# Optimization experiments

Hardware: AMD Instinct MI355X
Metric: run time of the kernel (lower is better)

Reference implementation:

```python
import jax, jax.numpy as jnp
import numpy as np

T = 8192        # total tokens
D = 2048        # hidden size
I = 2048        # intermediate dim
E = 8           # num experts
K = 2           # num_experts_per_tok


def setup_inputs() -> dict:
    key = jax.random.key(0)
    k1, k2, k3, k4, k5 = jax.random.split(key, 5)
    return {
        "inputs": jax.random.normal(k1, (T, D), dtype=jnp.float32),
        "router_logits": jax.random.normal(k2, (T, E), dtype=jnp.float32),
        "wi_0": jax.random.normal(k3, (E, D, I), dtype=jnp.float32) * 0.02,
        "wi_1": jax.random.normal(k4, (E, D, I), dtype=jnp.float32) * 0.02,
        "wo": jax.random.normal(k5, (E, I, D), dtype=jnp.float32) * 0.02,
    }


def reference(inputs, router_logits, wi_0, wi_1, wo):
    total_tokens, hidden = inputs.shape
    num_experts = router_logits.shape[-1]
    dtype = inputs.dtype

    # --- router: top-k, softmax over selected logits, renormalize ---
    top_k_logits, top_k_indices = jax.lax.top_k(router_logits, K)     # [T,K]
    top_k_weights = jax.nn.softmax(top_k_logits.astype(jnp.float32), axis=-1).astype(dtype)
    top_k_weights = top_k_weights / jnp.sum(top_k_weights, axis=-1, keepdims=True)

    # --- permute: replicate each token K times, sort token-expert pairs by expert id ---
    flat_experts = top_k_indices.reshape(-1)                          # [T*K]
    sort_idx = jnp.argsort(flat_experts)                              # stable sort -> grouped by expert
    x_rep = jnp.repeat(inputs, K, axis=0)                             # [T*K, D]
    x_sorted = x_rep[sort_idx]                                        # [T*K, D] grouped per expert
    group_sizes = jnp.bincount(flat_experts, length=num_experts).astype(jnp.int32)  # [E]

    # --- grouped GEMM (ragged_dot) over contiguous expert groups: SwiGLU FFN ---
    h0 = jax.lax.ragged_dot(x_sorted, wi_0, group_sizes, preferred_element_type=dtype)
    h1 = jax.lax.ragged_dot(x_sorted, wi_1, group_sizes, preferred_element_type=dtype)
    inter = jax.nn.silu(h0) * h1                                      # [T*K, I]
    out_sorted = jax.lax.ragged_dot(inter, wo, group_sizes, preferred_element_type=dtype)  # [T*K, D]

    # --- unpermute + weighted combine ---
    inv_idx = jnp.argsort(sort_idx)
    out_pairs = out_sorted[inv_idx].reshape(total_tokens, K, hidden)  # [T,K,D]
    output = jnp.einsum("tkd,tk->td", out_pairs, top_k_weights)       # [T,D]
    return output
```

## Files before the change

kernel.cpp:

```cpp
#include <hip/hip_runtime.h>
#include <hip/hip_bf16.h>
#include <stdint.h>

#define T_TOK 8192
#define DDIM 2048
#define IDIM 2048
#define NEXP 8
#define NPAIR (T_TOK*2)
#define MAXROWS (NPAIR + NEXP*128)
#define MAXTILES (MAXROWS/128)

typedef __attribute__((ext_vector_type(8))) short short8;
typedef __attribute__((ext_vector_type(4))) float f32x4;

__device__ __forceinline__ ushort f2bf(float f) {
  union { float f; unsigned int u; } v; v.f = f;
  unsigned int u = v.u;
  unsigned int r = (u + 0x7fffu + ((u >> 16) & 1u)) >> 16;
  return (ushort)r;
}

__device__ __forceinline__ void glds16(const void* g, void* l) {
  __builtin_amdgcn_global_load_lds(
      (const __attribute__((address_space(1))) unsigned int*)g,
      (__attribute__((address_space(3))) unsigned int*)l, 16, 0, 0);
}

__global__ void router_kernel(const float* __restrict__ logits, int* __restrict__ pair_e,
                              float* __restrict__ pair_w, int* __restrict__ cnt) {
  __shared__ int c[NEXP];
  int tid = threadIdx.x;
  int t = blockIdx.x * 256 + tid;
  if (tid < NEXP) c[tid] = 0;
  __syncthreads();
  float lv[NEXP];
  #pragma unroll
  for (int e = 0; e < NEXP; ++e) lv[e] = logits[t * NEXP + e];
  int i0 = 0;
  #pragma unroll
  for (int e = 1; e < NEXP; ++e) if (lv[e] > lv[i0]) i0 = e;
  int i1 = (i0 == 0) ? 1 : 0;
  #pragma unroll
  for (int e = 0; e < NEXP; ++e) if (e != i0 && lv[e] > lv[i1]) i1 = e;
  float ex = __expf(lv[i1] - lv[i0]);
  float w1 = ex / (1.f + ex);
  float w0 = 1.f - w1;
  pair_e[2*t] = i0; pair_e[2*t+1] = i1;
  pair_w[2*t] = w0; pair_w[2*t+1] = w1;
  atomicAdd(&c[i0], 1); atomicAdd(&c[i1], 1);
  __syncthreads();
  if (tid < NEXP) atomicAdd(&cnt[tid], c[tid]);
}

__global__ void scan_kernel(const int* __restrict__ cnt, int* __restrict__ poff) {
  if (threadIdx.x == 0 && blockIdx.x == 0) {
    int o = 0; poff[0] = 0;
    for (int e = 0; e < NEXP; ++e) { o += (cnt[e] + 127) & ~127; poff[e+1] = o; }
  }
}

__global__ void scatter_kernel(const int* __restrict__ pair_e, const float* __restrict__ pair_w,
                               const int* __restrict__ poff, int* __restrict__ fill,
                               int* __restrict__ row_token, float* __restrict__ row_weight) {
  __shared__ int lc[NEXP], lb[NEXP];
  int tid = threadIdx.x;
  int t = blockIdx.x * 256 + tid;
  if (tid < NEXP) lc[tid] = 0;
  __syncthreads();
  int e0 = pair_e[2*t], e1 = pair_e[2*t+1];
  int r0 = atomicAdd(&lc[e0], 1);
  int r1 = atomicAdd(&lc[e1], 1);
  __syncthreads();
  if (tid < NEXP) lb[tid] = atomicAdd(&fill[tid], lc[tid]);
  __syncthreads();
  int p0 = poff[e0] + lb[e0] + r0;
  int p1 = poff[e1] + lb[e1] + r1;
  row_token[p0] = t; row_weight[p0] = pair_w[2*t];
  row_token[p1] = t; row_weight[p1] = pair_w[2*t+1];
}

__global__ void convert_x_kernel(const float* __restrict__ x, ushort* __restrict__ xb) {
  size_t i = ((size_t)blockIdx.x * 256 + threadIdx.x) * 8;
  float4 a = *(const float4*)(x + i);
  float4 b = *(const float4*)(x + i + 4);
  uint4 o;
  o.x = (unsigned)f2bf(a.x) | ((unsigned)f2bf(a.y) << 16);
  o.y = (unsigned)f2bf(a.z) | ((unsigned)f2bf(a.w) << 16);
  o.z = (unsigned)f2bf(b.x) | ((unsigned)f2bf(b.y) << 16);
  o.w = (unsigned)f2bf(b.z) | ((unsigned)f2bf(b.w) << 16);
  *(uint4*)(xb + i) = o;
}

__global__ void transpose_w_kernel(const float* __restrict__ wi0, const float* __restrict__ wi1,
                                   const float* __restrict__ wo, ushort* __restrict__ w0t,
                                   ushort* __restrict__ w1t, ushort* __restrict__ wot) {
  int mz = blockIdx.z;
  int mat = mz >> 3, e = mz & 7;
  const float* src = (mat == 0 ? wi0 : (mat == 1 ? wi1 : wo)) + (size_t)e * DDIM * IDIM;
  ushort* dst = (mat == 0 ? w0t : (mat == 1 ? w1t : wot)) + (size_t)e * DDIM * IDIM;
  __shared__ ushort tbuf[64][72];
  int tid = threadIdx.x;
  int bi = blockIdx.x, bj = blockIdx.y;
  int rl = tid >> 4;
  int cl = (tid & 15) * 4;
  #pragma unroll
  for (int it = 0; it < 4; ++it) {
    int r = rl + it * 16;
    float4 v = *(const float4*)(src + (size_t)(bi*64 + r) * 2048 + bj*64 + cl);
    tbuf[cl+0][r] = f2bf(v.x);
    tbuf[cl+1][r] = f2bf(v.y);
    tbuf[cl+2][r] = f2bf(v.z);
    tbuf[cl+3][r] = f2bf(v.w);
  }
  __syncthreads();
  int n = tid >> 2, ch = tid & 3;
  const ushort* p = &tbuf[n][ch*16];
  unsigned pk[8];
  #pragma unroll
  for (int j = 0; j < 8; ++j) pk[j] = (unsigned)p[2*j] | ((unsigned)p[2*j+1] << 16);
  ushort* d = dst + (size_t)(bj*64 + n) * 2048 + bi*64 + ch*16;
  uint4 o0, o1;
  o0.x = pk[0]; o0.y = pk[1]; o0.z = pk[2]; o0.w = pk[3];
  o1.x = pk[4]; o1.y = pk[5]; o1.z = pk[6]; o1.w = pk[7];
  *(uint4*)(d) = o0;
  *(uint4*)(d + 8) = o1;
}

__global__ __launch_bounds__(256, 2) void gemm1_kernel(
    const ushort* __restrict__ xb, const ushort* __restrict__ w0t,
    const ushort* __restrict__ w1t, const int* __restrict__ row_token,
    const int* __restrict__ poff, ushort* __restrict__ inter) {
  const int rt = blockIdx.x, ct = blockIdx.y;
  const int row0 = rt * 128;
  if (row0 >= poff[NEXP]) return;
  int e = 0;
  #pragma unroll
  for (int i = 1; i < NEXP; ++i) e += (row0 >= poff[i]);

  __shared__ __align__(16) char smem[2 * 24576];
  const int tid = threadIdx.x;
  const int w = tid >> 6, l = tid & 63;

  const ushort* aSrc[2]; const ushort* b0Src[2]; const ushort* b1Src[2];
  int ldsOff[2];
  #pragma unroll
  for (int c = 0; c < 2; ++c) {
    int o = c * 4096 + w * 1024 + l * 16;
    int m = o >> 6;
    int ci = (o >> 4) & 3;
    int kl = ((ci ^ ((m >> 1) & 3)) << 3);
    ldsOff[c] = c * 4096 + w * 1024;
    int tok = row_token[row0 + m];
    aSrc[c]  = xb  + (size_t)tok * DDIM + kl;
    int n = ct * 128 + m;
    b0Src[c] = w0t + ((size_t)e * IDIM + n) * DDIM + kl;
    b1Src[c] = w1t + ((size_t)e * IDIM + n) * DDIM + kl;
  }

  f32x4 acc0[4][4], acc1[4][4];
  #pragma unroll
  for (int i = 0; i < 4; ++i)
    #pragma unroll
    for (int j = 0; j < 4; ++j) { acc0[i][j] = (f32x4)(0.f); acc1[i][j] = (f32x4)(0.f); }

  const int wr = w >> 1, wc = w & 1;
  const int fr = l & 15, kq = l >> 4;
  int aOff[4], bOff[4];
  #pragma unroll
  for (int mi = 0; mi < 4; ++mi) {
    int m = wr * 64 + mi * 16 + fr;
    aOff[mi] = m * 64 + ((kq * 16) ^ (((m >> 1) & 3) << 4));
  }
  #pragma unroll
  for (int ni = 0; ni < 4; ++ni) {
    int n = wc * 64 + ni * 16 + fr;
    bOff[ni] = n * 64 + ((kq * 16) ^ (((n >> 1) & 3) << 4));
  }

  const int NT = DDIM / 32;
  #pragma unroll
  for (int c = 0; c < 2; ++c) {
    glds16(aSrc[c],  smem + 0     + ldsOff[c]);
    glds16(b0Src[c], smem + 8192  + ldsOff[c]);
    glds16(b1Src[c], smem + 16384 + ldsOff[c]);
  }
  __syncthreads();

  int buf = 0;
  for (int kt = 0; kt < NT; ++kt) {
    if (kt + 1 < NT) {
      char* base = smem + (buf ^ 1) * 24576;
      int kadv = (kt + 1) * 32;
      #pragma unroll
      for (int c = 0; c < 2; ++c) {
        glds16(aSrc[c]  + kadv, base + 0     + ldsOff[c]);
        glds16(b0Src[c] + kadv, base + 8192  + ldsOff[c]);
        glds16(b1Src[c] + kadv, base + 16384 + ldsOff[c]);
      }
    }
    const char* cb = smem + buf * 24576;
    short8 a[4], b0[4], b1[4];
    #pragma unroll
    for (int mi = 0; mi < 4; ++mi) a[mi] = *(const short8*)(cb + aOff[mi]);
    #pragma unroll
    for (int ni = 0; ni < 4; ++ni) {
      b0[ni] = *(const short8*)(cb + 8192  + bOff[ni]);
      b1[ni] = *(const short8*)(cb + 16384 + bOff[ni]);
    }
    #pragma unroll
    for (int mi = 0; mi < 4; ++mi)
      #pragma unroll
      for (int ni = 0; ni < 4; ++ni) {
        acc0[mi][ni] = __builtin_amdgcn_mfma_f32_16x16x32_bf16(a[mi], b0[ni], acc0[mi][ni], 0, 0, 0);
        acc1[mi][ni] = __builtin_amdgcn_mfma_f32_16x16x32_bf16(a[mi], b1[ni], acc1[mi][ni], 0, 0, 0);
      }
    __syncthreads();
    buf ^= 1;
  }

  #pragma unroll
  for (int mi = 0; mi < 4; ++mi)
    #pragma unroll
    for (int ni = 0; ni < 4; ++ni) {
      int col = ct * 128 + wc * 64 + ni * 16 + fr;
      #pragma unroll
      for (int j = 0; j < 4; ++j) {
        int row = row0 + wr * 64 + mi * 16 + kq * 4 + j;
        float h0 = acc0[mi][ni][j];
        float h1 = acc1[mi][ni][j];
        float s = h0 / (1.f + __expf(-h0));
        inter[(size_t)row * IDIM + col] = f2bf(s * h1);
      }
    }
}

__global__ __launch_bounds__(256, 2) void gemm2_kernel(
    const ushort* __restrict__ inter, const ushort* __restrict__ wot,
    const int* __restrict__ row_token, const float* __restrict__ row_weight,
    const int* __restrict__ poff, float* __restrict__ dout) {
  const int rt = blockIdx.x, ct = blockIdx.y;
  const int row0 = rt * 128;
  if (row0 >= poff[NEXP]) return;
  int e = 0;
  #pragma unroll
  for (int i = 1; i < NEXP; ++i) e += (row0 >= poff[i]);

  __shared__ __align__(16) char smem[2 * 16384];
  __shared__ int tok_s[128];
  __shared__ float wgt_s[128];
  const int tid = threadIdx.x;
  if (tid < 128) { tok_s[tid] = row_token[row0 + tid]; wgt_s[tid] = row_weight[row0 + tid]; }

  const int w = tid >> 6, l = tid & 63;
  const ushort* aSrc[2]; const ushort* bSrc[2];
  int ldsOff[2];
  #pragma unroll
  for (int c = 0; c < 2; ++c) {
    int o = c * 4096 + w * 1024 + l * 16;
    int m = o >> 6;
    int ci = (o >> 4) & 3;
    int kl = ((ci ^ ((m >> 1) & 3)) << 3);
    ldsOff[c] = c * 4096 + w * 1024;
    aSrc[c] = inter + (size_t)(row0 + m) * IDIM + kl;
    bSrc[c] = wot + ((size_t)e * DDIM + ct * 128 + m) * IDIM + kl;
  }

  f32x4 acc[4][4];
  #pragma unroll
  for (int i = 0; i < 4; ++i)
    #pragma unroll
    for (int j = 0; j < 4; ++j) acc[i][j] = (f32x4)(0.f);

  const int wr = w >> 1, wc = w & 1;
  const int fr = l & 15, kq = l >> 4;
  int aOff[4], bOff[4];
  #pragma unroll
  for (int mi = 0; mi < 4; ++mi) {
    int m = wr * 64 + mi * 16 + fr;
    aOff[mi] = m * 64 + ((kq * 16) ^ (((m >> 1) & 3) << 4));
  }
  #pragma unroll
  for (int ni = 0; ni < 4; ++ni) {
    int n = wc * 64 + ni * 16 + fr;
    bOff[ni] = n * 64 + ((kq * 16) ^ (((n >> 1) & 3) << 4));
  }

  const int NT = IDIM / 32;
  #pragma unroll
  for (int c = 0; c < 2; ++c) {
    glds16(aSrc[c], smem + 0    + ldsOff[c]);
    glds16(bSrc[c], smem + 8192 + ldsOff[c]);
  }
  __syncthreads();

  int buf = 0;
  for (int kt = 0; kt < NT; ++kt) {
    if (kt + 1 < NT) {
      char* base = smem + (buf ^ 1) * 16384;
      int kadv = (kt + 1) * 32;
      #pragma unroll
      for (int c = 0; c < 2; ++c) {
        glds16(aSrc[c] + kadv, base + 0    + ldsOff[c]);
        glds16(bSrc[c] + kadv, base + 8192 + ldsOff[c]);
      }
    }
    const char* cb = smem + buf * 16384;
    short8 a[4], b[4];
    #pragma unroll
    for (int mi = 0; mi < 4; ++mi) a[mi] = *(const short8*)(cb + aOff[mi]);
    #pragma unroll
    for (int ni = 0; ni < 4; ++ni) b[ni] = *(const short8*)(cb + 8192 + bOff[ni]);
    #pragma unroll
    for (int mi = 0; mi < 4; ++mi)
      #pragma unroll
      for (int ni = 0; ni < 4; ++ni)
        acc[mi][ni] = __builtin_amdgcn_mfma_f32_16x16x32_bf16(a[mi], b[ni], acc[mi][ni], 0, 0, 0);
    __syncthreads();
    buf ^= 1;
  }

  #pragma unroll
  for (int mi = 0; mi < 4; ++mi)
    #pragma unroll
    for (int ni = 0; ni < 4; ++ni) {
      int col = ct * 128 + wc * 64 + ni * 16 + fr;
      #pragma unroll
      for (int j = 0; j < 4; ++j) {
        int rl2 = wr * 64 + mi * 16 + kq * 4 + j;
        float wv = wgt_s[rl2];
        if (wv != 0.f) {
          int t = tok_s[rl2];
          atomicAdd(&dout[(size_t)t * DDIM + col], wv * acc[mi][ni][j]);
        }
      }
    }
}

extern "C" void kernel_launch(void* const* d_in, const int* in_sizes, int n_in,
                              void* d_out, int out_size, void* d_ws, size_t ws_size,
                              hipStream_t stream) {
  const float* x   = (const float*)d_in[0];
  const float* rl  = (const float*)d_in[1];
  const float* wi0 = (const float*)d_in[2];
  const float* wi1 = (const float*)d_in[3];
  const float* wo  = (const float*)d_in[4];
  float* out = (float*)d_out;

  char* ws = (char*)d_ws;
  ushort* xb    = (ushort*)(ws);
  ushort* w0t   = (ushort*)(ws + 33554432ull);
  ushort* w1t   = (ushort*)(ws + 100663296ull);
  ushort* wot   = (ushort*)(ws + 167772160ull);
  ushort* inter = (ushort*)(ws + 234881024ull);
  char* ctrl    = ws + 306184192ull;
  int*   row_token  = (int*)(ctrl);
  float* row_weight = (float*)(ctrl + 69632);
  int*   cnt   = (int*)(ctrl + 139264);
  int*   fill  = (int*)(ctrl + 139296);
  int*   poff  = (int*)(ctrl + 139328);
  int*   pair_e = (int*)(ctrl + 139392);
  float* pair_w = (float*)(ctrl + 204928);

  hipMemsetAsync(ctrl, 0, 139328, stream);
  router_kernel<<<T_TOK/256, 256, 0, stream>>>(rl, pair_e, pair_w, cnt);
  scan_kernel<<<1, 64, 0, stream>>>(cnt, poff);
  scatter_kernel<<<T_TOK/256, 256, 0, stream>>>(pair_e, pair_w, poff, fill, row_token, row_weight);
  convert_x_kernel<<<(T_TOK*DDIM)/(256*8), 256, 0, stream>>>(x, xb);
  transpose_w_kernel<<<dim3(32, 32, 24), 256, 0, stream>>>(wi0, wi1, wo, w0t, w1t, wot);
  hipMemsetAsync(d_out, 0, (size_t)out_size * sizeof(float), stream);
  gemm1_kernel<<<dim3(MAXTILES, 16), 256, 0, stream>>>(xb, w0t, w1t, row_token, poff, inter);
  gemm2_kernel<<<dim3(MAXTILES, 16), 256, 0, stream>>>(inter, wot, row_token, row_weight, poff, out);
}
```

Baseline: 1.092 ms.

## Enlarge GEMM tiles to 256 rows with 512 threads and software-pipelined staging

Both grouped GEMMs move to 256-row tiles with 8 waves, 64-wide K steps, a larger LDS double buffer and staged async loads interleaved with MFMA phases under fine-grained vmcnt waits and s_setprio. Expert padding grows to 256 rows and the grid is reordered so column tiles vary fastest, which is meant to improve operand reuse and overlap loads with compute. The wo transpose is deferred until after gemm1 and reuses the w0t buffer, which shrinks the workspace. The costs are more padding rows, 128KB of LDS per block, and fragile hand-written barrier and waitcnt scheduling.

```diff
diff --git a/kernel.cpp b/kernel.cpp
--- a/kernel.cpp
+++ b/kernel.cpp
@@ -7,8 +7,9 @@
 #define IDIM 2048
 #define NEXP 8
 #define NPAIR (T_TOK*2)
-#define MAXROWS (NPAIR + NEXP*128)
-#define MAXTILES (MAXROWS/128)
+#define MAXROWS (NPAIR + NEXP*256)
+#define RTILES (MAXROWS/256)
+#define NTK 32
 
 typedef __attribute__((ext_vector_type(8))) short short8;
 typedef __attribute__((ext_vector_type(4))) float f32x4;
@@ -25,6 +26,11 @@
       (const __attribute__((address_space(1))) unsigned int*)g,
       (__attribute__((address_space(3))) unsigned int*)l, 16, 0, 0);
 }
+
+#define BAR() __builtin_amdgcn_s_barrier()
+#define VMC6() asm volatile("s_waitcnt vmcnt(6)" ::: "memory")
+#define VMC4() asm volatile("s_waitcnt vmcnt(4)" ::: "memory")
+#define VMC0() asm volatile("s_waitcnt vmcnt(0)" ::: "memory")
 
 __global__ void router_kernel(const float* __restrict__ logits, int* __restrict__ pair_e,
                               float* __restrict__ pair_w, int* __restrict__ cnt) {
@@ -55,7 +61,7 @@
 __global__ void scan_kernel(const int* __restrict__ cnt, int* __restrict__ poff) {
   if (threadIdx.x == 0 && blockIdx.x == 0) {
     int o = 0; poff[0] = 0;
-    for (int e = 0; e < NEXP; ++e) { o += (cnt[e] + 127) & ~127; poff[e+1] = o; }
+    for (int e = 0; e < NEXP; ++e) { o += (cnt[e] + 255) & ~255; poff[e+1] = o; }
   }
 }
 
@@ -91,13 +97,12 @@
   *(uint4*)(xb + i) = o;
 }
 
-__global__ void transpose_w_kernel(const float* __restrict__ wi0, const float* __restrict__ wi1,
-                                   const float* __restrict__ wo, ushort* __restrict__ w0t,
-                                   ushort* __restrict__ w1t, ushort* __restrict__ wot) {
+__global__ void transpose_w_kernel(const float* __restrict__ s0, ushort* __restrict__ d0,
+                                   const float* __restrict__ s1, ushort* __restrict__ d1) {
   int mz = blockIdx.z;
   int mat = mz >> 3, e = mz & 7;
-  const float* src = (mat == 0 ? wi0 : (mat == 1 ? wi1 : wo)) + (size_t)e * DDIM * IDIM;
-  ushort* dst = (mat == 0 ? w0t : (mat == 1 ? w1t : wot)) + (size_t)e * DDIM * IDIM;
+  const float* src = (mat ? s1 : s0) + (size_t)e * DDIM * IDIM;
+  ushort* dst = (mat ? d1 : d0) + (size_t)e * DDIM * IDIM;
   __shared__ ushort tbuf[64][72];
   int tid = threadIdx.x;
   int bi = blockIdx.x, bj = blockIdx.y;
@@ -126,211 +131,221 @@
   *(uint4*)(d + 8) = o1;
 }
 
-__global__ __launch_bounds__(256, 2) void gemm1_kernel(
+__global__ __launch_bounds__(512, 2) void gemm1_kernel(
     const ushort* __restrict__ xb, const ushort* __restrict__ w0t,
     const ushort* __restrict__ w1t, const int* __restrict__ row_token,
     const int* __restrict__ poff, ushort* __restrict__ inter) {
-  const int rt = blockIdx.x, ct = blockIdx.y;
-  const int row0 = rt * 128;
+  const int ct = blockIdx.x;
+  const int rt = blockIdx.y;
+  const int row0 = rt * 256;
   if (row0 >= poff[NEXP]) return;
   int e = 0;
   #pragma unroll
   for (int i = 1; i < NEXP; ++i) e += (row0 >= poff[i]);
 
-  __shared__ __align__(16) char smem[2 * 24576];
+  __shared__ __align__(16) char sm[131072];
   const int tid = threadIdx.x;
   const int w = tid >> 6, l = tid & 63;
-
-  const ushort* aSrc[2]; const ushort* b0Src[2]; const ushort* b1Src[2];
-  int ldsOff[2];
-  #pragma unroll
-  for (int c = 0; c < 2; ++c) {
-    int o = c * 4096 + w * 1024 + l * 16;
-    int m = o >> 6;
-    int ci = (o >> 4) & 3;
-    int kl = ((ci ^ ((m >> 1) & 3)) << 3);
-    ldsOff[c] = c * 4096 + w * 1024;
-    int tok = row_token[row0 + m];
-    aSrc[c]  = xb  + (size_t)tok * DDIM + kl;
-    int n = ct * 128 + m;
-    b0Src[c] = w0t + ((size_t)e * IDIM + n) * DDIM + kl;
-    b1Src[c] = w1t + ((size_t)e * IDIM + n) * DDIM + kl;
-  }
-
-  f32x4 acc0[4][4], acc1[4][4];
-  #pragma unroll
-  for (int i = 0; i < 4; ++i)
-    #pragma unroll
-    for (int j = 0; j < 4; ++j) { acc0[i][j] = (f32x4)(0.f); acc1[i][j] = (f32x4)(0.f); }
-
-  const int wr = w >> 1, wc = w & 1;
+  const int wr = w >> 2, wc = w & 3;
   const int fr = l & 15, kq = l >> 4;
-  int aOff[4], bOff[4];
-  #pragma unroll
-  for (int mi = 0; mi < 4; ++mi) {
-    int m = wr * 64 + mi * 16 + fr;
-    aOff[mi] = m * 64 + ((kq * 16) ^ (((m >> 1) & 3) << 4));
-  }
-  #pragma unroll
-  for (int ni = 0; ni < 4; ++ni) {
-    int n = wc * 64 + ni * 16 + fr;
-    bOff[ni] = n * 64 + ((kq * 16) ^ (((n >> 1) & 3) << 4));
-  }
-
-  const int NT = DDIM / 32;
-  #pragma unroll
-  for (int c = 0; c < 2; ++c) {
-    glds16(aSrc[c],  smem + 0     + ldsOff[c]);
-    glds16(b0Src[c], smem + 8192  + ldsOff[c]);
-    glds16(b1Src[c], smem + 16384 + ldsOff[c]);
-  }
-  __syncthreads();
-
-  int buf = 0;
-  for (int kt = 0; kt < NT; ++kt) {
-    if (kt + 1 < NT) {
-      char* base = smem + (buf ^ 1) * 24576;
-      int kadv = (kt + 1) * 32;
-      #pragma unroll
-      for (int c = 0; c < 2; ++c) {
-        glds16(aSrc[c]  + kadv, base + 0     + ldsOff[c]);
-        glds16(b0Src[c] + kadv, base + 8192  + ldsOff[c]);
-        glds16(b1Src[c] + kadv, base + 16384 + ldsOff[c]);
-      }
+
+  const int mloc = tid >> 3;
+  const int kl = ((tid & 7) ^ (mloc & 7)) << 3;
+  const ushort* aP[2][2]; const ushort* b0P[2]; const ushort* b1P[2];
+  #pragma unroll
+  for (int h = 0; h < 2; ++h)
+    #pragma unroll
+    for (int li = 0; li < 2; ++li) {
+      int tok = row_token[row0 + h*128 + li*64 + mloc];
+      aP[h][li] = xb + (size_t)tok * DDIM + kl;
     }
-    const char* cb = smem + buf * 24576;
-    short8 a[4], b0[4], b1[4];
-    #pragma unroll
-    for (int mi = 0; mi < 4; ++mi) a[mi] = *(const short8*)(cb + aOff[mi]);
-    #pragma unroll
-    for (int ni = 0; ni < 4; ++ni) {
-      b0[ni] = *(const short8*)(cb + 8192  + bOff[ni]);
-      b1[ni] = *(const short8*)(cb + 16384 + bOff[ni]);
-    }
-    #pragma unroll
-    for (int mi = 0; mi < 4; ++mi)
-      #pragma unroll
-      for (int ni = 0; ni < 4; ++ni) {
-        acc0[mi][ni] = __builtin_amdgcn_mfma_f32_16x16x32_bf16(a[mi], b0[ni], acc0[mi][ni], 0, 0, 0);
-        acc1[mi][ni] = __builtin_amdgcn_mfma_f32_16x16x32_bf16(a[mi], b1[ni], acc1[mi][ni], 0, 0, 0);
-      }
-    __syncthreads();
-    buf ^= 1;
-  }
-
-  #pragma unroll
-  for (int mi = 0; mi < 4; ++mi)
-    #pragma unroll
-    for (int ni = 0; ni < 4; ++ni) {
-      int col = ct * 128 + wc * 64 + ni * 16 + fr;
+  #pragma unroll
+  for (int li = 0; li < 2; ++li) {
+    int n = ct*128 + li*64 + mloc;
+    b0P[li] = w0t + ((size_t)e * IDIM + n) * DDIM + kl;
+    b1P[li] = w1t + ((size_t)e * IDIM + n) * DDIM + kl;
+  }
+  const int dOff = tid * 16;
+
+#define S_A(h, dd, tt) do { int ka = (tt)*64; char* db = sm + (dd)*65536 + (h)*16384 + dOff; \
+  glds16(aP[h][0] + ka, db); glds16(aP[h][1] + ka, db + 8192); } while(0)
+#define S_B0(dd, tt) do { int ka = (tt)*64; char* db = sm + (dd)*65536 + 32768 + dOff; \
+  glds16(b0P[0] + ka, db); glds16(b0P[1] + ka, db + 8192); } while(0)
+#define S_B1(dd, tt) do { int ka = (tt)*64; char* db = sm + (dd)*65536 + 49152 + dOff; \
+  glds16(b1P[0] + ka, db); glds16(b1P[1] + ka, db + 8192); } while(0)
+
+  const int pc0 = ((kq ^ (fr & 7)) << 4);
+  const int pc1 = (((4 + kq) ^ (fr & 7)) << 4);
+  const int aBase = wr*16384 + fr*128;
+  const int bBase = 32768 + (wc*32 + fr)*128;
+
+#define RD_A(mq) do { const char* p_ = cur + aBase + (mq)*8192; \
+  _Pragma("unroll") for (int mi = 0; mi < 4; ++mi) { \
+    a[mi][0] = *(const short8*)(p_ + mi*2048 + pc0); \
+    a[mi][1] = *(const short8*)(p_ + mi*2048 + pc1); } } while(0)
+#define RD_B(dst_, gg) do { const char* p_ = cur + bBase + (gg)*16384; \
+  _Pragma("unroll") for (int ni = 0; ni < 2; ++ni) { \
+    dst_[ni][0] = *(const short8*)(p_ + ni*2048 + pc0); \
+    dst_[ni][1] = *(const short8*)(p_ + ni*2048 + pc1); } } while(0)
+#define MM(accv, mq, bb) do { __builtin_amdgcn_s_setprio(1); \
+  _Pragma("unroll") for (int mi = 0; mi < 4; ++mi) \
+  _Pragma("unroll") for (int ni = 0; ni < 2; ++ni) { \
+    accv[(mq)*4+mi][ni] = __builtin_amdgcn_mfma_f32_16x16x32_bf16(a[mi][0], bb[ni][0], accv[(mq)*4+mi][ni], 0,0,0); \
+    accv[(mq)*4+mi][ni] = __builtin_amdgcn_mfma_f32_16x16x32_bf16(a[mi][1], bb[ni][1], accv[(mq)*4+mi][ni], 0,0,0); } \
+  __builtin_amdgcn_s_setprio(0); } while(0)
+
+  f32x4 acc0[8][2], acc1[8][2];
+  #pragma unroll
+  for (int i = 0; i < 8; ++i)
+    #pragma unroll
+    for (int j = 0; j < 2; ++j) { acc0[i][j] = (f32x4)(0.f); acc1[i][j] = (f32x4)(0.f); }
+  short8 a[4][2], b0v[2][2], b1v[2][2];
+
+  S_A(0,0,0); S_A(1,0,0); S_B0(0,0); S_B1(0,0);
+  S_B0(1,1); S_B1(1,1); S_A(0,1,1);
+  VMC6(); BAR();
+
+  for (int t = 0; t < NTK; ++t) {
+    const char* cur = sm + (t & 1) * 65536;
+    const int d = t & 1;
+    RD_A(0); RD_B(b0v, 0);
+    if (t+1 < NTK) S_A(1, d^1, t+1);
+    BAR(); MM(acc0, 0, b0v); BAR();
+    RD_B(b1v, 1);
+    if (t+2 < NTK) S_B0(d, t+2);
+    BAR(); MM(acc1, 0, b1v); BAR();
+    RD_A(1);
+    if (t+2 < NTK) S_B1(d, t+2);
+    BAR(); MM(acc1, 1, b1v); BAR();
+    if (t+2 < NTK) { S_A(0, d, t+2); VMC6(); } else { VMC0(); }
+    BAR(); MM(acc0, 1, b0v); BAR();
+  }
+#undef S_A
+#undef S_B0
+#undef S_B1
+#undef RD_A
+#undef RD_B
+#undef MM
+
+  #pragma unroll
+  for (int ai = 0; ai < 8; ++ai)
+    #pragma unroll
+    for (int ni = 0; ni < 2; ++ni) {
+      int col = ct*128 + wc*32 + ni*16 + fr;
       #pragma unroll
       for (int j = 0; j < 4; ++j) {
-        int row = row0 + wr * 64 + mi * 16 + kq * 4 + j;
-        float h0 = acc0[mi][ni][j];
-        float h1 = acc1[mi][ni][j];
+        int row = row0 + wr*128 + ai*16 + kq*4 + j;
+        float h0 = acc0[ai][ni][j], h1 = acc1[ai][ni][j];
         float s = h0 / (1.f + __expf(-h0));
         inter[(size_t)row * IDIM + col] = f2bf(s * h1);
       }
     }
 }
 
-__global__ __launch_bounds__(256, 2) void gemm2_kernel(
+__global__ __launch_bounds__(512, 2) void gemm2_kernel(
     const ushort* __restrict__ inter, const ushort* __restrict__ wot,
     const int* __restrict__ row_token, const float* __restrict__ row_weight,
     const int* __restrict__ poff, float* __restrict__ dout) {
-  const int rt = blockIdx.x, ct = blockIdx.y;
-  const int row0 = rt * 128;
+  const int ct = blockIdx.x;
+  const int rt = blockIdx.y;
+  const int row0 = rt * 256;
   if (row0 >= poff[NEXP]) return;
   int e = 0;
   #pragma unroll
   for (int i = 1; i < NEXP; ++i) e += (row0 >= poff[i]);
 
-  __shared__ __align__(16) char smem[2 * 16384];
-  __shared__ int tok_s[128];
-  __shared__ float wgt_s[128];
+  __shared__ __align__(16) char sm[131072];
+  __shared__ int tok_s[256];
+  __shared__ float wgt_s[256];
   const int tid = threadIdx.x;
-  if (tid < 128) { tok_s[tid] = row_token[row0 + tid]; wgt_s[tid] = row_weight[row0 + tid]; }
+  if (tid < 256) { tok_s[tid] = row_token[row0 + tid]; wgt_s[tid] = row_weight[row0 + tid]; }
 
   const int w = tid >> 6, l = tid & 63;
-  const ushort* aSrc[2]; const ushort* bSrc[2];
-  int ldsOff[2];
-  #pragma unroll
-  for (int c = 0; c < 2; ++c) {
-    int o = c * 4096 + w * 1024 + l * 16;
-    int m = o >> 6;
-    int ci = (o >> 4) & 3;
-    int kl = ((ci ^ ((m >> 1) & 3)) << 3);
-    ldsOff[c] = c * 4096 + w * 1024;
-    aSrc[c] = inter + (size_t)(row0 + m) * IDIM + kl;
-    bSrc[c] = wot + ((size_t)e * DDIM + ct * 128 + m) * IDIM + kl;
-  }
-
-  f32x4 acc[4][4];
-  #pragma unroll
-  for (int i = 0; i < 4; ++i)
+  const int wr = w >> 2, wc = w & 3;
+  const int fr = l & 15, kq = l >> 4;
+
+  const int mloc = tid >> 3;
+  const int kl = ((tid & 7) ^ (mloc & 7)) << 3;
+  const ushort* aP[2][2]; const ushort* bP[2][2];
+  #pragma unroll
+  for (int h = 0; h < 2; ++h)
+    #pragma unroll
+    for (int li = 0; li < 2; ++li) {
+      aP[h][li] = inter + (size_t)(row0 + h*128 + li*64 + mloc) * IDIM + kl;
+      int n = ct*256 + h*128 + li*64 + mloc;
+      bP[h][li] = wot + ((size_t)e * DDIM + n) * IDIM + kl;
+    }
+  const int dOff = tid * 16;
+
+#define S_A2(h, dd, tt) do { int ka = (tt)*64; char* db = sm + (dd)*65536 + (h)*16384 + dOff; \
+  glds16(aP[h][0] + ka, db); glds16(aP[h][1] + ka, db + 8192); } while(0)
+#define S_B2(h, dd, tt) do { int ka = (tt)*64; char* db = sm + (dd)*65536 + 32768 + (h)*16384 + dOff; \
+  glds16(bP[h][0] + ka, db); glds16(bP[h][1] + ka, db + 8192); } while(0)
+
+  const int pc0 = ((kq ^ (fr & 7)) << 4);
+  const int pc1 = (((4 + kq) ^ (fr & 7)) << 4);
+  const int aBase = wr*16384 + fr*128;
+  const int bBase = 32768 + (wc>>1)*16384 + ((wc&1)*64 + fr)*128;
+
+#define RD_A2(mq) do { const char* p_ = cur + aBase + (mq)*8192; \
+  _Pragma("unroll") for (int mi = 0; mi < 4; ++mi) { \
+    a[mi][0] = *(const short8*)(p_ + mi*2048 + pc0); \
+    a[mi][1] = *(const short8*)(p_ + mi*2048 + pc1); } } while(0)
+#define RD_B2(dst_, nq) do { const char* p_ = cur + bBase + (nq)*4096; \
+  _Pragma("unroll") for (int ni = 0; ni < 2; ++ni) { \
+    dst_[ni][0] = *(const short8*)(p_ + ni*2048 + pc0); \
+    dst_[ni][1] = *(const short8*)(p_ + ni*2048 + pc1); } } while(0)
+#define MM2(mq, nq, bb) do { __builtin_amdgcn_s_setprio(1); \
+  _Pragma("unroll") for (int mi = 0; mi < 4; ++mi) \
+  _Pragma("unroll") for (int ni = 0; ni < 2; ++ni) { \
+    acc[(mq)*4+mi][(nq)*2+ni] = __builtin_amdgcn_mfma_f32_16x16x32_bf16(a[mi][0], bb[ni][0], acc[(mq)*4+mi][(nq)*2+ni], 0,0,0); \
+    acc[(mq)*4+mi][(nq)*2+ni] = __builtin_amdgcn_mfma_f32_16x16x32_bf16(a[mi][1], bb[ni][1], acc[(mq)*4+mi][(nq)*2+ni], 0,0,0); } \
+  __builtin_amdgcn_s_setprio(0); } while(0)
+
+  f32x4 acc[8][4];
+  #pragma unroll
+  for (int i = 0; i < 8; ++i)
     #pragma unroll
     for (int j = 0; j < 4; ++j) acc[i][j] = (f32x4)(0.f);
-
-  const int wr = w >> 1, wc = w & 1;
-  const int fr = l & 15, kq = l >> 4;
-  int aOff[4], bOff[4];
-  #pragma unroll
-  for (int mi = 0; mi < 4; ++mi) {
-    int m = wr * 64 + mi * 16 + fr;
-    aOff[mi] = m * 64 + ((kq * 16) ^ (((m >> 1) & 3) << 4));
-  }
-  #pragma unroll
-  for (int ni = 0; ni < 4; ++ni) {
-    int n = wc * 64 + ni * 16 + fr;
-    bOff[ni] = n * 64 + ((kq * 16) ^ (((n >> 1) & 3) << 4));
-  }
-
-  const int NT = IDIM / 32;
-  #pragma unroll
-  for (int c = 0; c < 2; ++c) {
-    glds16(aSrc[c], smem + 0    + ldsOff[c]);
-    glds16(bSrc[c], smem + 8192 + ldsOff[c]);
-  }
-  __syncthreads();
-
-  int buf = 0;
-  for (int kt = 0; kt < NT; ++kt) {
-    if (kt + 1 < NT) {
-      char* base = smem + (buf ^ 1) * 16384;
-      int kadv = (kt + 1) * 32;
-      #pragma unroll
-      for (int c = 0; c < 2; ++c) {
-        glds16(aSrc[c] + kadv, base + 0    + ldsOff[c]);
-        glds16(bSrc[c] + kadv, base + 8192 + ldsOff[c]);
-      }
-    }
-    const char* cb = smem + buf * 16384;
-    short8 a[4], b[4];
-    #pragma unroll
-    for (int mi = 0; mi < 4; ++mi) a[mi] = *(const short8*)(cb + aOff[mi]);
-    #pragma unroll
-    for (int ni = 0; ni < 4; ++ni) b[ni] = *(const short8*)(cb + 8192 + bOff[ni]);
-    #pragma unroll
-    for (int mi = 0; mi < 4; ++mi)
-      #pragma unroll
-      for (int ni = 0; ni < 4; ++ni)
-        acc[mi][ni] = __builtin_amdgcn_mfma_f32_16x16x32_bf16(a[mi], b[ni], acc[mi][ni], 0, 0, 0);
-    __syncthreads();
-    buf ^= 1;
-  }
-
-  #pragma unroll
-  for (int mi = 0; mi < 4; ++mi)
-    #pragma unroll
-    for (int ni = 0; ni < 4; ++ni) {
-      int col = ct * 128 + wc * 64 + ni * 16 + fr;
+  short8 a[4][2], bv0[2][2], bv1[2][2];
+
+  S_A2(0,0,0); S_A2(1,0,0); S_B2(0,0,0); S_B2(1,0,0);
+  S_B2(0,1,1); S_B2(1,1,1);
+  VMC4(); BAR();
+
+  for (int t = 0; t < NTK; ++t) {
+    const char* cur = sm + (t & 1) * 65536;
+    const int d = t & 1;
+    RD_A2(0); RD_B2(bv0, 0);
+    if (t+1 < NTK) S_A2(0, d^1, t+1);
+    BAR(); MM2(0, 0, bv0); BAR();
+    RD_B2(bv1, 1);
+    if (t+1 < NTK) S_A2(1, d^1, t+1);
+    BAR(); MM2(0, 1, bv1); BAR();
+    RD_A2(1);
+    if (t+2 < NTK) S_B2(0, d, t+2);
+    BAR(); MM2(1, 1, bv1); BAR();
+    if (t+2 < NTK) { S_B2(1, d, t+2); VMC4(); } else { VMC0(); }
+    BAR(); MM2(1, 0, bv0); BAR();
+  }
+#undef S_A2
+#undef S_B2
+#undef RD_A2
+#undef RD_B2
+#undef MM2
+
+  #pragma unroll
+  for (int ai = 0; ai < 8; ++ai)
+    #pragma unroll
+    for (int aj = 0; aj < 4; ++aj) {
+      int col = ct*256 + wc*64 + aj*16 + fr;
       #pragma unroll
       for (int j = 0; j < 4; ++j) {
-        int rl2 = wr * 64 + mi * 16 + kq * 4 + j;
+        int rl2 = wr*128 + ai*16 + kq*4 + j;
         float wv = wgt_s[rl2];
         if (wv != 0.f) {
-          int t = tok_s[rl2];
-          atomicAdd(&dout[(size_t)t * DDIM + col], wv * acc[mi][ni][j]);
+          int tk = tok_s[rl2];
+          atomicAdd(&dout[(size_t)tk * DDIM + col], wv * acc[ai][aj][j]);
         }
       }
     }
@@ -350,24 +365,24 @@
   ushort* xb    = (ushort*)(ws);
   ushort* w0t   = (ushort*)(ws + 33554432ull);
   ushort* w1t   = (ushort*)(ws + 100663296ull);
-  ushort* wot   = (ushort*)(ws + 167772160ull);
-  ushort* inter = (ushort*)(ws + 234881024ull);
-  char* ctrl    = ws + 306184192ull;
+  ushort* inter = (ushort*)(ws + 167772160ull);
+  char* ctrl    = ws + 243269632ull;
   int*   row_token  = (int*)(ctrl);
-  float* row_weight = (float*)(ctrl + 69632);
-  int*   cnt   = (int*)(ctrl + 139264);
-  int*   fill  = (int*)(ctrl + 139296);
-  int*   poff  = (int*)(ctrl + 139328);
-  int*   pair_e = (int*)(ctrl + 139392);
-  float* pair_w = (float*)(ctrl + 204928);
-
-  hipMemsetAsync(ctrl, 0, 139328, stream);
+  float* row_weight = (float*)(ctrl + 73728);
+  int*   cnt   = (int*)(ctrl + 147456);
+  int*   fill  = (int*)(ctrl + 147488);
+  int*   poff  = (int*)(ctrl + 147520);
+  int*   pair_e = (int*)(ctrl + 147584);
+  float* pair_w = (float*)(ctrl + 213120);
+
+  hipMemsetAsync(ctrl, 0, 147520, stream);
   router_kernel<<<T_TOK/256, 256, 0, stream>>>(rl, pair_e, pair_w, cnt);
   scan_kernel<<<1, 64, 0, stream>>>(cnt, poff);
   scatter_kernel<<<T_TOK/256, 256, 0, stream>>>(pair_e, pair_w, poff, fill, row_token, row_weight);
   convert_x_kernel<<<(T_TOK*DDIM)/(256*8), 256, 0, stream>>>(x, xb);
-  transpose_w_kernel<<<dim3(32, 32, 24), 256, 0, stream>>>(wi0, wi1, wo, w0t, w1t, wot);
+  transpose_w_kernel<<<dim3(32, 32, 16), 256, 0, stream>>>(wi0, w0t, wi1, w1t);
   hipMemsetAsync(d_out, 0, (size_t)out_size * sizeof(float), stream);
-  gemm1_kernel<<<dim3(MAXTILES, 16), 256, 0, stream>>>(xb, w0t, w1t, row_token, poff, inter);
-  gemm2_kernel<<<dim3(MAXTILES, 16), 256, 0, stream>>>(inter, wot, row_token, row_weight, poff, out);
-}
+  gemm1_kernel<<<dim3(16, RTILES), 512, 0, stream>>>(xb, w0t, w1t, row_token, poff, inter);
+  transpose_w_kernel<<<dim3(32, 32, 8), 256, 0, stream>>>(wo, w0t, wo, w0t);
+  gemm2_kernel<<<dim3(8, RTILES), 512, 0, stream>>>(inter, w0t, row_token, row_weight, poff, out);
+}
```

Result: faster. 985.9 us (-9.8%).
